# Kernel optimization log

Hardware: AMD Instinct MI355X
Metric: run time of the kernel (lower is better)

The kernel has to match this reference:

```python
import jax, jax.numpy as jnp
import numpy as np

D_E, D_ENC, D_DEC, H = 128, 256, 512, 8
HD = D_DEC // H
B, S, T, V, C = 32, 128, 128, 32000, 2


def gru_cell(x, h, Wih, Whh, bih, bhh):
    # PyTorch GRU cell: gates ordered (reset, update, new)
    gi = x @ Wih.T + bih
    gh = h @ Whh.T + bhh
    ir, iz, inn = jnp.split(gi, 3, axis=-1)
    hr, hz, hn = jnp.split(gh, 3, axis=-1)
    r = jax.nn.sigmoid(ir + hr)
    z = jax.nn.sigmoid(iz + hz)
    n = jnp.tanh(inn + r * hn)
    return (1.0 - z) * n + z * h


def setup_inputs():
    key = jax.random.key(0)
    ks = iter(jax.random.split(key, 40))
    def nrm(shape, s=0.05):
        return jax.random.normal(next(ks), shape, jnp.float32) * s
    inp = {}
    inp["nx"] = jax.random.randint(next(ks), (B, S), 0, V)
    inp["x"] = jax.random.randint(next(ks), (B, T), 0, V)
    inp["label"] = jax.random.randint(next(ks), (B,), 0, C)
    inp["tok_emb"] = nrm((V, D_E))
    inp["start_emb"] = nrm((1, D_E))
    inp["style_emb"] = nrm((C, D_DEC))
    for d in ("f", "b"):
        inp["enc_Wih_" + d] = nrm((3 * D_ENC, D_E))
        inp["enc_Whh_" + d] = nrm((3 * D_ENC, D_ENC))
        inp["enc_bih_" + d] = nrm((3 * D_ENC,))
        inp["enc_bhh_" + d] = nrm((3 * D_ENC,))
    inp["dec_Wih"] = nrm((3 * D_DEC, D_E))
    inp["dec_Whh"] = nrm((3 * D_DEC, D_DEC))
    inp["dec_bih"] = nrm((3 * D_DEC,))
    inp["dec_bhh"] = nrm((3 * D_DEC,))
    inp["attn_in_w"] = nrm((3 * D_DEC, D_DEC))
    inp["attn_in_b"] = nrm((3 * D_DEC,))
    inp["attn_out_w"] = nrm((D_DEC, D_DEC))
    inp["attn_out_b"] = nrm((D_DEC,))
    inp["ln_g"] = jnp.ones((D_DEC,), jnp.float32)
    inp["ln_b"] = jnp.zeros((D_DEC,), jnp.float32)
    inp["proj_w"] = nrm((V, D_DEC))
    inp["proj_b"] = nrm((V,))
    return inp


def _forward(nx, x, label, tok_emb, start_emb, style_emb,
             enc_Wih_f, enc_Whh_f, enc_bih_f, enc_bhh_f,
             enc_Wih_b, enc_Whh_b, enc_bih_b, enc_bhh_b,
             dec_Wih, dec_Whh, dec_bih, dec_bhh,
             attn_in_w, attn_in_b, attn_out_w, attn_out_b,
             ln_g, ln_b, proj_w, proj_b):
    b, s = nx.shape
    # --- bidirectional GRU encoder (dropout in eval mode => identity) ---
    emb = tok_emb[nx]                          # [B,S,dE]
    xs = jnp.swapaxes(emb, 0, 1)               # [S,B,dE]
    h0 = jnp.zeros((b, D_ENC), emb.dtype)

    def step_f(h, xt):
        h2 = gru_cell(xt, h, enc_Wih_f, enc_Whh_f, enc_bih_f, enc_bhh_f)
        return h2, h2

    def step_b(h, xt):
        h2 = gru_cell(xt, h, enc_Wih_b, enc_Whh_b, enc_bih_b, enc_bhh_b)
        return h2, h2

    _, out_f = jax.lax.scan(step_f, h0, xs)
    _, out_b = jax.lax.scan(step_b, h0, xs, reverse=True)
    memory = jnp.concatenate([out_f, out_b], axis=-1)   # [S,B,dDec] (seq-first, matches torch MHA)

    # --- precompute K/V projections of memory (invariant across decode steps) ---
    Wq, Wk, Wv = jnp.split(attn_in_w, 3, axis=0)
    bq, bk, bv = jnp.split(attn_in_b, 3)
    k = (memory @ Wk.T + bk).reshape(s, b, H, HD).transpose(1, 2, 0, 3)  # [B,H,S,HD]
    v = (memory @ Wv.T + bv).reshape(s, b, H, HD).transpose(1, 2, 0, 3)

    # --- teacher-forced decoder inputs: <start>, x[:,0], ..., x[:,T-2] ---
    dec_in = jnp.concatenate(
        [jnp.broadcast_to(start_emb[None, :, :], (b, 1, D_E)), tok_emb[x[:, :-1]]], axis=1)
    dec_xs = jnp.swapaxes(dec_in, 0, 1)        # [T,B,dE]
    h_init = style_emb[label]                  # [B,dDec]
    scale = 1.0 / np.sqrt(HD).astype(np.float32)

    def dec_step(h, xt):
        h_dec = gru_cell(xt, h, dec_Wih, dec_Whh, dec_bih, dec_bhh)      # [B,dDec]
        q = (h_dec @ Wq.T + bq).reshape(b, H, HD)
        scores = jnp.einsum('bhd,bhsd->bhs', q, k) * scale
        attn = jax.nn.softmax(scores, axis=-1)
        ctx = jnp.einsum('bhs,bhsd->bhd', attn, v).reshape(b, D_DEC)
        c = ctx @ attn_out_w.T + attn_out_b
        y = h_dec + c
        mu = jnp.mean(y, axis=-1, keepdims=True)
        var = jnp.var(y, axis=-1, keepdims=True)
        h_new = (y - mu) / jnp.sqrt(var + 1e-5) * ln_g + ln_b            # LayerNorm
        logits = h_new @ proj_w.T + proj_b                               # [B,V]
        return h_new, logits

    _, logits = jax.lax.scan(dec_step, h_init, dec_xs)   # [T,B,V]
    return jnp.swapaxes(logits, 0, 1)                    # [B,T,V]


def reference(nx, x, label, tok_emb, start_emb, style_emb,
              enc_Wih_f, enc_Whh_f, enc_bih_f, enc_bhh_f,
              enc_Wih_b, enc_Whh_b, enc_bih_b, enc_bhh_b,
              dec_Wih, dec_Whh, dec_bih, dec_bhh,
              attn_in_w, attn_in_b, attn_out_w, attn_out_b,
              ln_g, ln_b, proj_w, proj_b):
    return _forward(nx, x, label, tok_emb, start_emb, style_emb,
                    enc_Wih_f, enc_Whh_f, enc_bih_f, enc_bhh_f,
                    enc_Wih_b, enc_Whh_b, enc_bih_b, enc_bhh_b,
                    dec_Wih, dec_Whh, dec_bih, dec_bhh,
                    attn_in_w, attn_in_b, attn_out_w, attn_out_b,
                    ln_g, ln_b, proj_w, proj_b)
```

## Files before the change

### kernel.cpp

```cpp
#include <hip/hip_runtime.h>
#include <math.h>

typedef float f4 __attribute__((ext_vector_type(4)));
typedef short short8 __attribute__((ext_vector_type(8)));
typedef unsigned short us4 __attribute__((ext_vector_type(4)));

#define DEV static __device__ __forceinline__
#define AGENT __HIP_MEMORY_SCOPE_AGENT

DEV float bf2f(unsigned short u){ unsigned int x=((unsigned int)u)<<16; float f; __builtin_memcpy(&f,&x,4); return f; }
DEV unsigned short f2bf(float f){ unsigned int x; __builtin_memcpy(&x,&f,4); return (unsigned short)((x + 0x7fffu + ((x>>16)&1u))>>16); }

struct bfpair { short hi, lo; };
DEV bfpair splitbf(float v){
  bfpair p;
  unsigned short h_ = f2bf(v);
  p.hi = (short)h_;
  p.lo = (short)f2bf(v - bf2f(h_));
  return p;
}

DEV unsigned long long ldA64(const void* p){
  return __hip_atomic_load((const unsigned long long*)p, __ATOMIC_RELAXED, AGENT);
}
DEV void f2of(unsigned long long q, float* f0, float* f1){
  unsigned int lo=(unsigned int)q, hi=(unsigned int)(q>>32);
  __builtin_memcpy(f0,&lo,4); __builtin_memcpy(f1,&hi,4);
}

DEV void ld8x16_sc(const void* p, f4* o){
  asm volatile(
    "global_load_dwordx4 %0, %8, off sc0 sc1\n\t"
    "global_load_dwordx4 %1, %8, off offset:16 sc0 sc1\n\t"
    "global_load_dwordx4 %2, %8, off offset:32 sc0 sc1\n\t"
    "global_load_dwordx4 %3, %8, off offset:48 sc0 sc1\n\t"
    "global_load_dwordx4 %4, %8, off offset:64 sc0 sc1\n\t"
    "global_load_dwordx4 %5, %8, off offset:80 sc0 sc1\n\t"
    "global_load_dwordx4 %6, %8, off offset:96 sc0 sc1\n\t"
    "global_load_dwordx4 %7, %8, off offset:112 sc0 sc1\n\t"
    "s_waitcnt vmcnt(0)"
    : "=&v"(o[0]),"=&v"(o[1]),"=&v"(o[2]),"=&v"(o[3]),
      "=&v"(o[4]),"=&v"(o[5]),"=&v"(o[6]),"=&v"(o[7])
    : "v"(p) : "memory");
}
DEV void ld16x16_sc(const void* p, f4* o){
  asm volatile(
    "global_load_dwordx4 %0, %16, off sc0 sc1\n\t"
    "global_load_dwordx4 %1, %16, off offset:16 sc0 sc1\n\t"
    "global_load_dwordx4 %2, %16, off offset:32 sc0 sc1\n\t"
    "global_load_dwordx4 %3, %16, off offset:48 sc0 sc1\n\t"
    "global_load_dwordx4 %4, %16, off offset:64 sc0 sc1\n\t"
    "global_load_dwordx4 %5, %16, off offset:80 sc0 sc1\n\t"
    "global_load_dwordx4 %6, %16, off offset:96 sc0 sc1\n\t"
    "global_load_dwordx4 %7, %16, off offset:112 sc0 sc1\n\t"
    "global_load_dwordx4 %8, %16, off offset:128 sc0 sc1\n\t"
    "global_load_dwordx4 %9, %16, off offset:144 sc0 sc1\n\t"
    "global_load_dwordx4 %10, %16, off offset:160 sc0 sc1\n\t"
    "global_load_dwordx4 %11, %16, off offset:176 sc0 sc1\n\t"
    "global_load_dwordx4 %12, %16, off offset:192 sc0 sc1\n\t"
    "global_load_dwordx4 %13, %16, off offset:208 sc0 sc1\n\t"
    "global_load_dwordx4 %14, %16, off offset:224 sc0 sc1\n\t"
    "global_load_dwordx4 %15, %16, off offset:240 sc0 sc1\n\t"
    "s_waitcnt vmcnt(0)"
    : "=&v"(o[0]),"=&v"(o[1]),"=&v"(o[2]),"=&v"(o[3]),
      "=&v"(o[4]),"=&v"(o[5]),"=&v"(o[6]),"=&v"(o[7]),
      "=&v"(o[8]),"=&v"(o[9]),"=&v"(o[10]),"=&v"(o[11]),
      "=&v"(o[12]),"=&v"(o[13]),"=&v"(o[14]),"=&v"(o[15])
    : "v"(p) : "memory");
}
DEV void st8x16_sc(void* p, const f4* v){
  asm volatile(
    "global_store_dwordx4 %8, %0, off sc0 sc1\n\t"
    "global_store_dwordx4 %8, %1, off offset:16 sc0 sc1\n\t"
    "global_store_dwordx4 %8, %2, off offset:32 sc0 sc1\n\t"
    "global_store_dwordx4 %8, %3, off offset:48 sc0 sc1\n\t"
    "global_store_dwordx4 %8, %4, off offset:64 sc0 sc1\n\t"
    "global_store_dwordx4 %8, %5, off offset:80 sc0 sc1\n\t"
    "global_store_dwordx4 %8, %6, off offset:96 sc0 sc1\n\t"
    "global_store_dwordx4 %8, %7, off offset:112 sc0 sc1\n\t"
    "s_waitcnt vmcnt(0)"
    :: "v"(v[0]),"v"(v[1]),"v"(v[2]),"v"(v[3]),
       "v"(v[4]),"v"(v[5]),"v"(v[6]),"v"(v[7]),"v"(p) : "memory");
}

DEV int lds_off(int row,int strideShorts,int kShort){
  return row*strideShorts*2 + ((((kShort & ~7)*2) ^ ((row & 7)<<4)) + (kShort & 7)*2);
}
DEV void st8(unsigned short* lds,int row,int strideShorts,int k0,short8 v){
  *(short8*)((char*)lds + lds_off(row,strideShorts,k0)) = v;
}
DEV short8 ldfrag(const unsigned short* lds,int rowBase,int strideShorts,int k0){
  int lane = (int)(threadIdx.x & 63u);
  int row = rowBase + (lane & 15);
  int k = k0 + (lane >> 4)*8;
  return *(const short8*)((const char*)lds + lds_off(row,strideShorts,k));
}

DEV float dot8(f4 a0, f4 a1, short8 w){
  return a0[0]*bf2f((unsigned short)w[0]) + a0[1]*bf2f((unsigned short)w[1])
       + a0[2]*bf2f((unsigned short)w[2]) + a0[3]*bf2f((unsigned short)w[3])
       + a1[0]*bf2f((unsigned short)w[4]) + a1[1]*bf2f((unsigned short)w[5])
       + a1[2]*bf2f((unsigned short)w[6]) + a1[3]*bf2f((unsigned short)w[7]);
}

DEV void gbar_slot(int* slot, int nwg){
  __syncthreads();
  if (threadIdx.x==0){
    __hip_atomic_fetch_add(slot,1,__ATOMIC_RELAXED,AGENT);
    while (__hip_atomic_load(slot,__ATOMIC_RELAXED,AGENT) < nwg){
      __builtin_amdgcn_s_sleep(2);
    }
  }
  __syncthreads();
}

DEV void dbar(int* ctrs, int wg, int target){
  __syncthreads();
  if (threadIdx.x < 64){
    if (threadIdx.x == 0)
      __hip_atomic_store(&ctrs[wg*32], target, __ATOMIC_RELAXED, AGENT);
    for(;;){
      int v = __hip_atomic_load(&ctrs[(int)threadIdx.x*32], __ATOMIC_RELAXED, AGENT);
      if (__all(v >= target)) break;
      __builtin_amdgcn_s_sleep(2);
    }
  }
  __syncthreads();
}
DEV void vwait(int* ctrs, int target){
  if (threadIdx.x < 64){
    for(;;){
      int v = __hip_atomic_load(&ctrs[(int)threadIdx.x*32], __ATOMIC_RELAXED, AGENT);
      if (__all(v >= target)) break;
      __builtin_amdgcn_s_sleep(32);
    }
  }
  __syncthreads();
}
DEV void cwait(int* cctrs, int target){
  if (threadIdx.x < 64){
    for(;;){
      int v = __hip_atomic_load(&cctrs[((int)threadIdx.x & 7)*32], __ATOMIC_RELAXED, AGENT);
      if (__all(v >= target)) break;
      __builtin_amdgcn_s_sleep(32);
    }
  }
  __syncthreads();
}

__global__ void cvt_kernel(const float* __restrict__ src, unsigned short* __restrict__ dst, int n4){
  int stride = gridDim.x*blockDim.x;
  for (long i = blockIdx.x*blockDim.x + threadIdx.x; i < n4; i += stride){
    f4 v = *(const f4*)(src + i*4);
    us4 o; o[0]=f2bf(v[0]); o[1]=f2bf(v[1]); o[2]=f2bf(v[2]); o[3]=f2bf(v[3]);
    *(us4*)(dst + i*4) = o;
  }
}

__global__ void embed_kernel(const int* __restrict__ nx, const int* __restrict__ x,
  const int* __restrict__ label, const float* __restrict__ tok,
  const float* __restrict__ start, const float* __restrict__ style,
  unsigned short* __restrict__ embE, unsigned short* __restrict__ embD,
  float* __restrict__ h0)
{
  const int half = 4096*32;
  int i = blockIdx.x*256 + threadIdx.x;
  if (i < 2*half){
    const bool dec = i >= half;
    int j = dec ? i - half : i;
    int m = j >> 5, c4 = j & 31;
    int b = m & 31, tt = m >> 5;
    const float* src;
    if (!dec) src = tok + (long)nx[b*128 + tt]*128;
    else src = (tt == 0) ? start : (tok + (long)x[b*128 + tt - 1]*128);
    f4 v = *(const f4*)(src + c4*4);
    us4 o; o[0]=f2bf(v[0]); o[1]=f2bf(v[1]); o[2]=f2bf(v[2]); o[3]=f2bf(v[3]);
    *(us4*)((dec ? embD : embE) + (long)m*128 + c4*4) = o;
  } else {
    int j = i - 2*half;
    if (j < 4096){
      int b = j >> 7, c4 = j & 127;
      *(f4*)(h0 + b*512 + c4*4) = *(const f4*)(style + (long)label[b]*512 + c4*4);
    }
  }
}

__global__ void kv_reshape(const float* __restrict__ kvp, unsigned short* __restrict__ Kb, unsigned short* __restrict__ Vb){
  long i = (long)blockIdx.x*256 + threadIdx.x;
  if (i >= (long)4096*1024) return;
  int m = (int)(i >> 10), n = (int)(i & 1023);
  int s = m >> 5, b = m & 31;
  unsigned short bv = f2bf(kvp[i]);
  if (n < 512){
    int hh = n >> 6, d = n & 63;
    Kb[((long)(b*8 + hh)*128 + s)*64 + d] = bv;
  } else {
    int n2 = n - 512; int hh = n2 >> 6, d = n2 & 63;
    Vb[((long)(b*8 + hh)*64 + d)*128 + s] = bv;
  }
}

template<int MODE>
__global__ __launch_bounds__(256,2) void gemm64(
  const unsigned short* __restrict__ Bw, const float* __restrict__ bias,
  float* __restrict__ C, int M, int N, int K, int ldC,
  const unsigned short* __restrict__ Abf,
  const float* __restrict__ Af0, const float* __restrict__ Af1)
{
  __shared__ unsigned short a_s[64*64];
  __shared__ unsigned short b_s[64*64];
  const int tid = threadIdx.x, lane = tid & 63, wv = tid >> 6;
  const long mb = (long)blockIdx.x*64, nb = (long)blockIdx.y*64;
  f4 z = {0.f,0.f,0.f,0.f};
  f4 acc[4] = {z,z,z,z};
  const int r = tid >> 2, q = tid & 3, k0 = q*16;
  for (int kb = 0; kb < K; kb += 64){
    if (MODE==0){
      const unsigned short* src = Abf + (mb + r)*K + kb + k0;
      st8(a_s, r, 64, k0,   *(const short8*)src);
      st8(a_s, r, 64, k0+8, *(const short8*)(src+8));
    } else {
      float tmp[16];
      long m = mb + r;
      int kg = kb + k0;
      const float* base = (kg < 256) ? (Af0 + m*256 + kg) : (Af1 + m*256 + (kg - 256));
      #pragma unroll
      for (int i=0;i<16;i++) tmp[i] = base[i];
      short8 v0, v1;
      #pragma unroll
      for (int i=0;i<8;i++){ v0[i] = (short)f2bf(tmp[i]); v1[i] = (short)f2bf(tmp[8+i]); }
      st8(a_s, r, 64, k0, v0); st8(a_s, r, 64, k0+8, v1);
    }
    {
      const unsigned short* src = Bw + (nb + r)*K + kb + k0;
      st8(b_s, r, 64, k0,   *(const short8*)src);
      st8(b_s, r, 64, k0+8, *(const short8*)(src+8));
    }
    __syncthreads();
    #pragma unroll
    for (int kf=0; kf<2; kf++){
      short8 bfr = ldfrag(b_s, wv*16, 64, kf*32);
      #pragma unroll
      for (int mt=0; mt<4; mt++){
        short8 afr = ldfrag(a_s, mt*16, 64, kf*32);
        acc[mt] = __builtin_amdgcn_mfma_f32_16x16x32_bf16(afr, bfr, acc[mt], 0,0,0);
      }
    }
    __syncthreads();
  }
  const long col = nb + wv*16 + (lane & 15);
  const float bs = bias[col];
  #pragma unroll
  for (int mt=0; mt<4; mt++){
    #pragma unroll
    for (int rr=0; rr<4; rr++){
      long row = mb + mt*16 + (lane>>4)*4 + rr;
      C[row*(long)ldC + col] = acc[mt][rr] + bs;
    }
  }
}

__global__ __launch_bounds__(384) void enc_kernel(
  const float* __restrict__ WhhF_f, const float* __restrict__ WhhB_f,
  const float* __restrict__ GIF, const float* __restrict__ GIB,
  const float* __restrict__ bhhF, const float* __restrict__ bhhB,
  float* __restrict__ OUTF, float* __restrict__ OUTB,
  float* __restrict__ Hf,
  int* bar)
{
  __shared__ unsigned short whh_hi[96*256];
  __shared__ unsigned short whh_lo[96*256];
  __shared__ unsigned short a_hi[32*256];
  __shared__ unsigned short a_lo[32*256];
  __shared__ float ghscr[32*96];
  const int tid = threadIdx.x;
  const int wg = blockIdx.x;
  const int dir = wg >> 3, wgl = wg & 7;
  const float* Whh_f = dir ? WhhB_f : WhhF_f;
  const float* GI = dir ? GIB : GIF;
  const float* bhh = dir ? bhhB : bhhF;
  float* OUT = dir ? OUTB : OUTF;

  for (int idx = tid; idx < 96*32; idx += 384){
    int lr = idx >> 5, ch = idx & 31;
    int g_ = lr >> 5, jj = lr & 31;
    const float* wsrc = Whh_f + (long)(g_*256 + wgl*32 + jj)*256 + ch*8;
    short8 vh, vl;
    #pragma unroll
    for (int i=0;i<8;i++){ bfpair p = splitbf(wsrc[i]); vh[i] = p.hi; vl[i] = p.lo; }
    st8(whh_hi, lr, 256, ch*8, vh);
    st8(whh_lo, lr, 256, ch*8, vl);
  }
  __syncthreads();
  for (int t = 0; t < 128; t++){
    const int s = dir ? (127 - t) : t;
    const float* hbr = Hf + ((size_t)((t&1)*2 + dir))*(32*256);
    float* hbw = Hf + ((size_t)(((t+1)&1)*2 + dir))*(32*256);
    if (tid < 256){
      int b = tid >> 3, kg = tid & 7;
      const unsigned long long* hs = (const unsigned long long*)(hbr + b*256 + kg*32);
      #pragma unroll
      for (int c=0;c<4;c++){
        short8 vh, vl;
        #pragma unroll
        for (int i2=0;i2<4;i2++){
          unsigned long long qv = ldA64(hs + c*4 + i2);
          float f0, f1; f2of(qv, &f0, &f1);
          bfpair p0 = splitbf(f0), p1 = splitbf(f1);
          vh[i2*2] = p0.hi; vl[i2*2] = p0.lo;
          vh[i2*2+1] = p1.hi; vl[i2*2+1] = p1.lo;
        }
        st8(a_hi, b, 256, kg*32 + c*8, vh);
        st8(a_lo, b, 256, kg*32 + c*8, vl);
      }
    }
    __syncthreads();
    {
      const int wv = tid >> 6;
      f4 acc0 = {0.f,0.f,0.f,0.f}, acc1 = {0.f,0.f,0.f,0.f};
      #pragma unroll
      for (int kf=0; kf<8; kf++){
        short8 bhi = ldfrag(whh_hi, wv*16, 256, kf*32);
        short8 blo = ldfrag(whh_lo, wv*16, 256, kf*32);
        short8 ah0 = ldfrag(a_hi, 0, 256, kf*32);
        short8 al0 = ldfrag(a_lo, 0, 256, kf*32);
        short8 ah1 = ldfrag(a_hi, 16, 256, kf*32);
        short8 al1 = ldfrag(a_lo, 16, 256, kf*32);
        acc0 = __builtin_amdgcn_mfma_f32_16x16x32_bf16(ah0, bhi, acc0, 0,0,0);
        acc0 = __builtin_amdgcn_mfma_f32_16x16x32_bf16(al0, bhi, acc0, 0,0,0);
        acc0 = __builtin_amdgcn_mfma_f32_16x16x32_bf16(ah0, blo, acc0, 0,0,0);
        acc1 = __builtin_amdgcn_mfma_f32_16x16x32_bf16(ah1, bhi, acc1, 0,0,0);
        acc1 = __builtin_amdgcn_mfma_f32_16x16x32_bf16(al1, bhi, acc1, 0,0,0);
        acc1 = __builtin_amdgcn_mfma_f32_16x16x32_bf16(ah1, blo, acc1, 0,0,0);
      }
      const int lane = tid & 63;
      const int cl = wv*16 + (lane & 15);
      #pragma unroll
      for (int rr=0; rr<4; rr++){
        int r0 = (lane>>4)*4 + rr;
        ghscr[r0*96 + cl] = acc0[rr];
        ghscr[(16+r0)*96 + cl] = acc1[rr];
      }
    }
    __syncthreads();
    for (int task = tid; task < 1024; task += 384){
      int b = task >> 5, jj = task & 31;
      int jg = wgl*32 + jj;
      float ghr = ghscr[b*96 + jj]      + bhh[jg];
      float ghz = ghscr[b*96 + 32 + jj] + bhh[256 + jg];
      float ghn = ghscr[b*96 + 64 + jj] + bhh[512 + jg];
      const float* gi = GI + ((long)s*32 + b)*768;
      float r_ = 1.f/(1.f + __expf(-(gi[jg] + ghr)));
      float z_ = 1.f/(1.f + __expf(-(gi[256+jg] + ghz)));
      float n_ = tanhf(gi[512+jg] + r_*ghn);
      float hp = __hip_atomic_load(&hbr[b*256 + jg], __ATOMIC_RELAXED, AGENT);
      float hn = (1.f - z_)*n_ + z_*hp;
      OUT[((long)s*32 + b)*256 + jg] = hn;
      __hip_atomic_store(&hbw[b*256 + jg], hn, __ATOMIC_RELAXED, AGENT);
    }
    gbar_slot(bar + dir*128 + t, 8);
  }
}

struct DecS {
  unsigned short whh_hi[32*512];
  unsigned short whh_lo[32*512];
  unsigned short a_hi[32*512];
  unsigned short a_lo[32*512];
  float scr[32*64];
  float attn_l[4*128];
  float ctxs[4*64];
  float redm[32*8*2];
  float murs[64];
  float hnfr[32*8];
  float lngl[512], lnbl[512];
  float s1l[24], s2l[24];
};
struct VocS {
  unsigned short a_s[128*512];
  unsigned short b_s[64*64];
  float gl[512];
  float s2g[176];
};
struct CvtS {
  float redm[32*8*2];
  float murs[64];
};
union SU { DecS d; VocS v; CvtS c; };

__global__ __launch_bounds__(256,1) void dec_fused(
  const float* __restrict__ Whh_f,
  const unsigned short* __restrict__ WqBf,
  const unsigned short* __restrict__ Wout,
  const unsigned short* __restrict__ Kbf,
  const unsigned short* __restrict__ Vbf,
  const float* __restrict__ GI,
  const float* __restrict__ bhh,
  const float* __restrict__ aib,
  const float* __restrict__ aob,
  const float* __restrict__ lng,
  const float* __restrict__ lnb,
  const float* __restrict__ h0,
  float* __restrict__ Y,
  unsigned int* __restrict__ hdec32,
  unsigned short* __restrict__ Ybf,
  const unsigned short* __restrict__ Pbf,
  const float* __restrict__ projWf,
  const float* __restrict__ projB,
  float* __restrict__ out,
  int* ctrs)
{
  __shared__ SU s;
  const int tid = threadIdx.x;
  const int lane = tid & 63, wv = tid >> 6;
  int* cctrs = ctrs + 2048;

  if (blockIdx.x < 64){
    const int wg = blockIdx.x;
    const int h = wg >> 3, bg = wg & 7;
    const int jbase = wg*8;
    const int cw = wg & 7;

    if (tid < 24){ s.d.s1l[tid] = 0.f; s.d.s2l[tid] = 0.f; }
    __syncthreads();
    for (int idx = tid; idx < 32*64; idx += 256){
      int lr = idx >> 6, ch = idx & 63;
      short8 vh = {0,0,0,0,0,0,0,0}, vl = {0,0,0,0,0,0,0,0};
      if (lr < 24){
        int g_ = lr >> 3, jj = lr & 7;
        const float* wsrc = Whh_f + (long)(g_*512 + jbase + jj)*512 + ch*8;
        float s1p = 0.f, s2p = 0.f;
        #pragma unroll
        for (int i=0;i<8;i++){
          float wvv = wsrc[i];
          float gv = lng[ch*8+i];
          float bv = lnb[ch*8+i];
          float wp = wvv*gv;
          bfpair p = splitbf(wp);
          vh[i] = p.hi; vl[i] = p.lo;
          s1p += wp; s2p += bv*wvv;
        }
        atomicAdd(&s.d.s1l[lr], s1p);
        atomicAdd(&s.d.s2l[lr], s2p);
      }
      st8(s.d.whh_hi, lr, 512, ch*8, vh);
      st8(s.d.whh_lo, lr, 512, ch*8, vl);
    }
    for (int i = tid; i < 512; i += 256){ s.d.lngl[i] = lng[i]; s.d.lnbl[i] = lnb[i]; }

    const int qrow = h*64 + wv*16 + (lane & 15);
    const int kb0q = (lane>>4)*8;
    const unsigned short* wqbase = WqBf + (long)qrow*512 + kb0q;
    const int b_l = wv;
    const int bglob = bg*4 + b_l;
    const unsigned short* kbase = Kbf + ((long)(bglob*8 + h)*128 + lane*2)*64;
    const unsigned short* vbase = Vbf + ((long)(bglob*8 + h)*64 + lane)*128;
    const int jp = tid & 127;
    const unsigned short* wobase = Wout + (long)(jp*4)*512 + h*64;
    const float qb = aib[h*64 + wv*16 + (lane & 15)];
    const int bA = tid >> 3, kgA = tid & 7;
    const int jjA = tid & 7;
    const int jgA = jbase + jjA;
    const float bhr = bhh[jgA], bhz = bhh[512 + jgA], bhn = bhh[1024 + jgA];
    const float aobv = aob[jgA];
    __syncthreads();

    int lgen = 0;
    for (int t = 0; t < 128; t++){
      float gir = GI[((long)t*32 + bA)*1536 + jgA];
      float giz = GI[((long)t*32 + bA)*1536 + 512 + jgA];
      float gin = GI[((long)t*32 + bA)*1536 + 1024 + jgA];
      if (t == 0){
        const float* src = h0 + bA*512 + kgA*64;
        #pragma unroll
        for (int c=0;c<8;c++){
          short8 vh, vl;
          #pragma unroll
          for (int i=0;i<8;i++){
            float v = src[c*8+i];
            float gv = s.d.lngl[kgA*64 + c*8 + i];
            bfpair p = splitbf(v/gv);
            vh[i] = p.hi; vl[i] = p.lo;
            if (kgA == h && c == cw) s.d.hnfr[bA*8+i] = v;
          }
          st8(s.d.a_hi, bA, 512, kgA*64 + c*8, vh);
          st8(s.d.a_lo, bA, 512, kgA*64 + c*8, vl);
        }
        __syncthreads();
      } else {
        f4 yv[16];
        ld16x16_sc(Y + ((long)(t-1)*32 + bA)*512 + kgA*64, yv);
        float sm = 0.f, sq = 0.f;
        #pragma unroll
        for (int c=0;c<8;c++){
          short8 vh, vl;
          #pragma unroll
          for (int e=0;e<8;e++){
            float f = yv[c*2 + (e>>2)][e&3];
            sm += f; sq += f*f;
            bfpair p = splitbf(f);
            vh[e] = p.hi; vl[e] = p.lo;
            if (kgA == h && c == cw) s.d.hnfr[bA*8+e] = f;
          }
          st8(s.d.a_hi, bA, 512, kgA*64 + c*8, vh);
          st8(s.d.a_lo, bA, 512, kgA*64 + c*8, vl);
        }
        s.d.redm[(bA*8+kgA)*2] = sm; s.d.redm[(bA*8+kgA)*2+1] = sq;
        __syncthreads();
        if (tid < 32){
          float S1=0.f, S2=0.f;
          #pragma unroll
          for (int i=0;i<8;i++){ S1 += s.d.redm[(tid*8+i)*2]; S2 += s.d.redm[(tid*8+i)*2+1]; }
          float mu = S1*(1.f/512.f);
          float var = S2*(1.f/512.f) - mu*mu;
          s.d.murs[tid*2] = mu; s.d.murs[tid*2+1] = rsqrtf(var + 1e-5f);
        }
        __syncthreads();
      }
      {
        const int mt = wv >> 1, nt = wv & 1;
        f4 acc = {0.f,0.f,0.f,0.f};
        #pragma unroll
        for (int kf=0; kf<16; kf++){
          short8 bhi = ldfrag(s.d.whh_hi, nt*16, 512, kf*32);
          short8 blo = ldfrag(s.d.whh_lo, nt*16, 512, kf*32);
          short8 ahi = ldfrag(s.d.a_hi, mt*16, 512, kf*32);
          short8 alo = ldfrag(s.d.a_lo, mt*16, 512, kf*32);
          acc = __builtin_amdgcn_mfma_f32_16x16x32_bf16(ahi, bhi, acc, 0,0,0);
          acc = __builtin_amdgcn_mfma_f32_16x16x32_bf16(alo, bhi, acc, 0,0,0);
          acc = __builtin_amdgcn_mfma_f32_16x16x32_bf16(ahi, blo, acc, 0,0,0);
        }
        const int cl = nt*16 + (lane & 15);
        if (cl < 24){
          #pragma unroll
          for (int rr=0; rr<4; rr++){
            int row = mt*16 + (lane>>4)*4 + rr;
            s.d.scr[row*32 + cl] = acc[rr];
          }
        }
      }
      __syncthreads();
      {
        const float mu = t ? s.d.murs[bA*2] : 0.f;
        const float rsv = t ? s.d.murs[bA*2+1] : 1.f;
        const float c2 = rsv*mu;
        float ghr = rsv*s.d.scr[bA*32 + jjA]      - c2*s.d.s1l[jjA]      + (t ? s.d.s2l[jjA]      : 0.f) + bhr;
        float ghz = rsv*s.d.scr[bA*32 + 8 + jjA]  - c2*s.d.s1l[8 + jjA]  + (t ? s.d.s2l[8 + jjA]  : 0.f) + bhz;
        float ghn = rsv*s.d.scr[bA*32 + 16 + jjA] - c2*s.d.s1l[16 + jjA] + (t ? s.d.s2l[16 + jjA] : 0.f) + bhn;
        float r_ = 1.f/(1.f + __expf(-(gir + ghr)));
        float z_ = 1.f/(1.f + __expf(-(giz + ghz)));
        float n_ = tanhf(gin + r_*ghn);
        float hpv = s.d.hnfr[bA*8 + jjA];
        float hp = t ? (hpv - mu)*rsv*s.d.lngl[jgA] + s.d.lnbl[jgA] : hpv;
        float hd = (1.f - z_)*n_ + z_*hp;
        unsigned int hb = (unsigned int)f2bf(hd);
        unsigned int other = (unsigned int)__shfl_xor((int)hb, 1);
        if ((jjA & 1) == 0){
          unsigned int pack = hb | (other << 16);
          __hip_atomic_store(&hdec32[bA*256 + (jgA >> 1)], pack, __ATOMIC_RELAXED, AGENT);
        }
        __hip_atomic_store(&Y[((long)t*32 + bA)*512 + jgA], hd + aobv, __ATOMIC_RELAXED, AGENT);
      }
      dbar(ctrs, wg, ++lgen);
      {
        f4 hv[8];
        ld8x16_sc(hdec32 + bA*256 + kgA*32, hv);
        #pragma unroll
        for (int c=0;c<8;c++){
          short8 v;
          #pragma unroll
          for (int w2=0; w2<4; w2++){
            float fv = hv[c][w2];
            unsigned int u; __builtin_memcpy(&u, &fv, 4);
            v[w2*2]   = (short)(u & 0xffff);
            v[w2*2+1] = (short)(u >> 16);
          }
          st8(s.d.a_hi, bA, 512, kgA*64 + c*8, v);
        }
      }
      __syncthreads();
      {
        f4 acc0 = {0.f,0.f,0.f,0.f}, acc1 = {0.f,0.f,0.f,0.f};
        #pragma unroll
        for (int kf=0; kf<16; kf++){
          short8 bfr = *(const short8*)(wqbase + kf*32);
          acc0 = __builtin_amdgcn_mfma_f32_16x16x32_bf16(ldfrag(s.d.a_hi, 0, 512, kf*32), bfr, acc0, 0,0,0);
          acc1 = __builtin_amdgcn_mfma_f32_16x16x32_bf16(ldfrag(s.d.a_hi, 16, 512, kf*32), bfr, acc1, 0,0,0);
        }
        const int cl = wv*16 + (lane & 15);
        #pragma unroll
        for (int rr=0; rr<4; rr++){
          int r0 = (lane>>4)*4 + rr;
          s.d.scr[r0*64 + cl] = acc0[rr] + qb;
          s.d.scr[(16+r0)*64 + cl] = acc1[rr] + qb;
        }
      }
      __syncthreads();
      {
        const f4* qp = (const f4*)(s.d.scr + bglob*64);
        float s0 = 0.f, s1 = 0.f;
        #pragma unroll
        for (int c=0;c<8;c++) s0 += dot8(qp[c*2], qp[c*2+1], *(const short8*)(kbase + c*8));
        #pragma unroll
        for (int c=0;c<8;c++) s1 += dot8(qp[c*2], qp[c*2+1], *(const short8*)(kbase + 64 + c*8));
        s0 *= 0.125f; s1 *= 0.125f;
        float mx = fmaxf(s0, s1);
        #pragma unroll
        for (int o=1;o<64;o<<=1) mx = fmaxf(mx, __shfl_xor(mx, o));
        float e0 = __expf(s0 - mx), e1 = __expf(s1 - mx);
        float sm = e0 + e1;
        #pragma unroll
        for (int o=1;o<64;o<<=1) sm += __shfl_xor(sm, o);
        float inv = 1.f/sm;
        s.d.attn_l[b_l*128 + lane*2]   = e0*inv;
        s.d.attn_l[b_l*128 + lane*2+1] = e1*inv;
      }
      __syncthreads();
      {
        const f4* ap = (const f4*)(s.d.attn_l + b_l*128);
        float cx = 0.f;
        #pragma unroll
        for (int c=0;c<16;c++) cx += dot8(ap[c*2], ap[c*2+1], *(const short8*)(vbase + c*8));
        s.d.ctxs[b_l*64 + lane] = cx;
      }
      __syncthreads();
      {
        const int b2 = tid >> 7;
        #pragma unroll
        for (int jj=0;jj<4;jj++){
          const unsigned short* wb = wobase + (long)jj*512;
          short8 w0 = *(const short8*)(wb);
          short8 w1 = *(const short8*)(wb+8);
          short8 w2 = *(const short8*)(wb+16);
          short8 w3 = *(const short8*)(wb+24);
          short8 w4 = *(const short8*)(wb+32);
          short8 w5 = *(const short8*)(wb+40);
          short8 w6 = *(const short8*)(wb+48);
          short8 w7 = *(const short8*)(wb+56);
          #pragma unroll
          for (int bb=0; bb<2; bb++){
            const int bl = b2 + bb*2;
            const int bgl = bg*4 + bl;
            const f4* cp = (const f4*)(s.d.ctxs + bl*64);
            float cj = dot8(cp[0], cp[1], w0) + dot8(cp[2], cp[3], w1)
                     + dot8(cp[4], cp[5], w2) + dot8(cp[6], cp[7], w3)
                     + dot8(cp[8], cp[9], w4) + dot8(cp[10], cp[11], w5)
                     + dot8(cp[12], cp[13], w6) + dot8(cp[14], cp[15], w7);
            atomicAdd(&Y[((long)t*32 + bgl)*512 + jp*4 + jj], cj);
          }
        }
      }
      dbar(ctrs, wg, ++lgen);
    }
  } else if (blockIdx.x < 72){
    const int w = blockIdx.x - 64;
    const int rr = tid >> 3, seg = tid & 7;
    for (int c = 0; c < 16; c++){
      vwait(ctrs, 16*(c+1));
      long m = (long)c*256 + w*32 + rr;
      f4 yv[16];
      ld16x16_sc(Y + m*512 + seg*64, yv);
      float sm = 0.f, sq = 0.f;
      #pragma unroll
      for (int i=0;i<16;i++){
        f4 v = yv[i];
        sm += v[0]+v[1]+v[2]+v[3];
        sq += v[0]*v[0]+v[1]*v[1]+v[2]*v[2]+v[3]*v[3];
      }
      s.c.redm[(rr*8+seg)*2] = sm; s.c.redm[(rr*8+seg)*2+1] = sq;
      __syncthreads();
      if (tid < 32){
        float S1=0.f, S2=0.f;
        #pragma unroll
        for (int i=0;i<8;i++){ S1 += s.c.redm[(tid*8+i)*2]; S2 += s.c.redm[(tid*8+i)*2+1]; }
        float mu = S1*(1.f/512.f);
        float var = S2*(1.f/512.f) - mu*mu;
        s.c.murs[tid*2] = mu; s.c.murs[tid*2+1] = rsqrtf(var + 1e-5f);
      }
      __syncthreads();
      const float mu = s.c.murs[rr*2], rsv = s.c.murs[rr*2+1];
      f4 ob[8];
      #pragma unroll
      for (int i2=0;i2<32;i2++){
        float a0 = (yv[(2*i2)>>2][(2*i2)&3] - mu)*rsv;
        float a1v = (yv[(2*i2+1)>>2][(2*i2+1)&3] - mu)*rsv;
        unsigned int u = (unsigned int)f2bf(a0) | ((unsigned int)f2bf(a1v)<<16);
        float uf; __builtin_memcpy(&uf,&u,4);
        ob[i2>>2][i2&3] = uf;
      }
      st8x16_sc(Ybf + m*512 + seg*64, ob);
      __syncthreads();
      if (tid == 0)
        __hip_atomic_store(&cctrs[w*32], c+1, __ATOMIC_RELAXED, AGENT);
    }
  } else {
    const int w2 = blockIdx.x - 72;
    const int c0 = w2*174;
    const int cn = (32000 - c0 < 174) ? (32000 - c0) : 174;
    for (int cc = tid; cc < 176; cc += 256){
      if (cc < cn){
        const float* pw = projWf + (long)(c0+cc)*512;
        float s2 = 0.f;
        for (int k=0;k<512;k++) s2 += lnb[k]*pw[k];
        s.v.s2g[cc] = s2;
      }
    }
    for (int i = tid; i < 512; i += 256) s.v.gl[i] = lng[i];
    __syncthreads();
    const f4 z4 = {0.f,0.f,0.f,0.f};
    for (int c=0; c<16; c++){
      cwait(cctrs, c+1);
      for (int half=0; half<2; half++){
        const long rbase = (long)c*256 + half*128;
        {
          const int row = tid >> 1, seg = tid & 1;
          const unsigned short* src = Ybf + (rbase + row)*512 + seg*256;
          #pragma unroll
          for (int blk=0; blk<2; blk++){
            f4 av[16];
            ld16x16_sc(src + blk*128, av);
            #pragma unroll
            for (int i=0;i<16;i++){
              f4 tv = av[i];
              short8 s8; __builtin_memcpy(&s8, &tv, 16);
              st8(s.v.a_s, row, 512, seg*256 + blk*128 + i*8, s8);
            }
          }
        }
        __syncthreads();
        for (int nt=0; nt<3; nt++){
          f4 acc[8] = {z4,z4,z4,z4,z4,z4,z4,z4};
          for (int kt=0; kt<8; kt++){
            {
              const int r = tid >> 2, q = tid & 3, k0 = q*16;
              const int col = nt*64 + r;
              short8 v0 = {0,0,0,0,0,0,0,0}, v1 = {0,0,0,0,0,0,0,0};
              if (col < cn){
                const unsigned short* src = Pbf + (long)(c0+col)*512 + kt*64 + k0;
                #pragma unroll
                for (int i=0;i<8;i++){
                  v0[i] = (short)f2bf(bf2f(src[i])   * s.v.gl[kt*64 + k0 + i]);
                  v1[i] = (short)f2bf(bf2f(src[8+i]) * s.v.gl[kt*64 + k0 + 8 + i]);
                }
              }
              st8(s.v.b_s, r, 64, k0, v0);
              st8(s.v.b_s, r, 64, k0+8, v1);
            }
            __syncthreads();
            #pragma unroll
            for (int kf=0; kf<2; kf++){
              short8 bfr = ldfrag(s.v.b_s, wv*16, 64, kf*32);
              #pragma unroll
              for (int mt=0; mt<8; mt++){
                short8 afr = ldfrag(s.v.a_s, mt*16, 512, kt*64 + kf*32);
                acc[mt] = __builtin_amdgcn_mfma_f32_16x16x32_bf16(afr, bfr, acc[mt], 0,0,0);
              }
            }
            __syncthreads();
          }
          const int colloc = nt*64 + wv*16 + (lane & 15);
          if (colloc < cn){
            const int vcol = c0 + colloc;
            const float corr = s.v.s2g[colloc] + projB[vcol];
            #pragma unroll
            for (int mt=0; mt<8; mt++){
              #pragma unroll
              for (int rr=0; rr<4; rr++){
                int rowl = mt*16 + (lane>>4)*4 + rr;
                long m = rbase + rowl;
                long tt = m >> 5, b = m & 31;
                out[(b*128 + tt)*32000 + vcol] = acc[mt][rr] + corr;
              }
            }
          }
        }
        __syncthreads();
      }
    }
  }
}

extern "C" void kernel_launch(void* const* d_in, const int* in_sizes, int n_in,
                              void* d_out, int out_size, void* d_ws, size_t ws_size,
                              hipStream_t stream)
{
  const int* nx = (const int*)d_in[0];
  const int* x = (const int*)d_in[1];
  const int* label = (const int*)d_in[2];
  const float* tok = (const float*)d_in[3];
  const float* start = (const float*)d_in[4];
  const float* style = (const float*)d_in[5];
  const float* eWihF = (const float*)d_in[6];
  const float* eWhhF = (const float*)d_in[7];
  const float* ebihF = (const float*)d_in[8];
  const float* ebhhF = (const float*)d_in[9];
  const float* eWihB = (const float*)d_in[10];
  const float* eWhhB = (const float*)d_in[11];
  const float* ebihB = (const float*)d_in[12];
  const float* ebhhB = (const float*)d_in[13];
  const float* dWih = (const float*)d_in[14];
  const float* dWhh = (const float*)d_in[15];
  const float* dbih = (const float*)d_in[16];
  const float* dbhh = (const float*)d_in[17];
  const float* ainW = (const float*)d_in[18];
  const float* ainB = (const float*)d_in[19];
  const float* aoutW = (const float*)d_in[20];
  const float* aoutB = (const float*)d_in[21];
  const float* lng = (const float*)d_in[22];
  const float* lnb = (const float*)d_in[23];
  const float* projW = (const float*)d_in[24];
  const float* projB = (const float*)d_in[25];
  float* out = (float*)d_out;
  char* W = (char*)d_ws;

  size_t off = 0;
  auto alloc = [&](size_t sz){ size_t o = off; off = (off + sz + 255) & ~(size_t)255; return o; };
  const size_t O_HF   = alloc(4*32*256*4);
  const size_t O_BAR  = alloc(16384);
  const size_t O_EIHF = alloc(768*128*2);
  const size_t O_EIHB = alloc(768*128*2);
  const size_t O_DIH  = alloc(1536*128*2);
  const size_t O_AIN  = alloc(1536*512*2);
  const size_t O_AOUT = alloc(512*512*2);
  const size_t O_PROJ = alloc((size_t)32000*512*2);
  const size_t O_EMBE = alloc(4096*128*2);
  const size_t O_EMBD = alloc(4096*128*2);
  const size_t O_KBF  = alloc((size_t)32*8*128*64*2);
  const size_t O_VBF  = alloc((size_t)32*8*128*64*2);
  const size_t O_HDEC = alloc(32*256*4);
  const size_t O_YBF  = alloc((size_t)4096*512*2);
  const size_t O_GIF  = alloc((size_t)4096*768*4);
  const size_t O_GIB  = alloc((size_t)4096*768*4);
  const size_t O_GID  = alloc((size_t)4096*1536*4);
  const size_t O_OUTF = alloc((size_t)4096*256*4);
  const size_t O_OUTB = alloc((size_t)4096*256*4);
  const size_t O_KVP  = alloc((size_t)4096*1024*4);
  const size_t O_Y    = alloc((size_t)4096*512*4);
  const size_t O_H0   = alloc(32*512*4);

  (void)hipMemsetAsync(W + O_HF, 0, (O_BAR - O_HF) + 16384, stream);

  auto US = [&](size_t o){ return (unsigned short*)(W + o); };
  auto FP = [&](size_t o){ return (float*)(W + o); };

  {
    const struct { const float* s; size_t d; int n; } cvs[] = {
      {eWihF, O_EIHF, 768*128}, {eWihB, O_EIHB, 768*128},
      {dWih,  O_DIH,  1536*128},
      {ainW,  O_AIN,  1536*512}, {aoutW, O_AOUT, 512*512},
      {projW, O_PROJ, 32000*512},
    };
    for (auto &c : cvs){
      int n4 = c.n/4;
      int blocks = (n4 + 255)/256; if (blocks > 4096) blocks = 4096;
      cvt_kernel<<<blocks, 256, 0, stream>>>(c.s, US(c.d), n4);
    }
  }
  embed_kernel<<<1040, 256, 0, stream>>>(nx, x, label, tok, start, style,
                                         US(O_EMBE), US(O_EMBD), FP(O_H0));
  gemm64<0><<<dim3(64,12), 256, 0, stream>>>(US(O_EIHF), ebihF, FP(O_GIF), 4096, 768, 128, 768,
                                             US(O_EMBE), nullptr, nullptr);
  gemm64<0><<<dim3(64,12), 256, 0, stream>>>(US(O_EIHB), ebihB, FP(O_GIB), 4096, 768, 128, 768,
                                             US(O_EMBE), nullptr, nullptr);
  gemm64<0><<<dim3(64,24), 256, 0, stream>>>(US(O_DIH), dbih, FP(O_GID), 4096, 1536, 128, 1536,
                                             US(O_EMBD), nullptr, nullptr);
  enc_kernel<<<16, 384, 0, stream>>>(eWhhF, eWhhB, FP(O_GIF), FP(O_GIB),
                                     ebhhF, ebhhB, FP(O_OUTF), FP(O_OUTB), FP(O_HF),
                                     (int*)(W + O_BAR) + 3072);
  gemm64<1><<<dim3(64,16), 256, 0, stream>>>(US(O_AIN) + 512*512, ainB + 512, FP(O_KVP),
                                             4096, 1024, 512, 1024,
                                             nullptr, FP(O_OUTF), FP(O_OUTB));
  kv_reshape<<<16384, 256, 0, stream>>>(FP(O_KVP), US(O_KBF), US(O_VBF));
  dec_fused<<<256, 256, 0, stream>>>(dWhh, US(O_AIN), US(O_AOUT), US(O_KBF), US(O_VBF),
                                     FP(O_GID), dbhh, ainB, aoutB, lng, lnb, FP(O_H0),
                                     FP(O_Y), (unsigned int*)(W + O_HDEC), US(O_YBF),
                                     US(O_PROJ), projW, projB, out,
                                     (int*)(W + O_BAR));
  (void)in_sizes; (void)n_in; (void)out_size; (void)ws_size;
}
```

Baseline: 4.503 ms.

## Compute attention queries only for the block's own batches and prefetch GI

```diff
diff --git a/kernel.cpp b/kernel.cpp
--- a/kernel.cpp
+++ b/kernel.cpp
@@ -28,6 +28,12 @@
   __builtin_memcpy(f0,&lo,4); __builtin_memcpy(f1,&hi,4);
 }
 
+DEV void ld1x16_sc(const void* p, f4* o){
+  asm volatile(
+    "global_load_dwordx4 %0, %1, off sc0 sc1\n\t"
+    "s_waitcnt vmcnt(0)"
+    : "=&v"(o[0]) : "v"(p) : "memory");
+}
 DEV void ld8x16_sc(const void* p, f4* o){
   asm volatile(
     "global_load_dwordx4 %0, %8, off sc0 sc1\n\t"
@@ -132,7 +138,7 @@
     for(;;){
       int v = __hip_atomic_load(&ctrs[(int)threadIdx.x*32], __ATOMIC_RELAXED, AGENT);
       if (__all(v >= target)) break;
-      __builtin_amdgcn_s_sleep(32);
+      __builtin_amdgcn_s_sleep(64);
     }
   }
   __syncthreads();
@@ -142,7 +148,7 @@
     for(;;){
       int v = __hip_atomic_load(&cctrs[((int)threadIdx.x & 7)*32], __ATOMIC_RELAXED, AGENT);
       if (__all(v >= target)) break;
-      __builtin_amdgcn_s_sleep(32);
+      __builtin_amdgcn_s_sleep(64);
     }
   }
   __syncthreads();
@@ -466,10 +472,10 @@
     __syncthreads();
 
     int lgen = 0;
+    float gir = GI[((long)0*32 + bA)*1536 + jgA];
+    float giz = GI[((long)0*32 + bA)*1536 + 512 + jgA];
+    float gin = GI[((long)0*32 + bA)*1536 + 1024 + jgA];
     for (int t = 0; t < 128; t++){
-      float gir = GI[((long)t*32 + bA)*1536 + jgA];
-      float giz = GI[((long)t*32 + bA)*1536 + 512 + jgA];
-      float gin = GI[((long)t*32 + bA)*1536 + 1024 + jgA];
       if (t == 0){
         const float* src = h0 + bA*512 + kgA*64;
         #pragma unroll
@@ -563,41 +569,37 @@
       }
       dbar(ctrs, wg, ++lgen);
       {
-        f4 hv[8];
-        ld8x16_sc(hdec32 + bA*256 + kgA*32, hv);
-        #pragma unroll
-        for (int c=0;c<8;c++){
-          short8 v;
-          #pragma unroll
-          for (int w2=0; w2<4; w2++){
-            float fv = hv[c][w2];
-            unsigned int u; __builtin_memcpy(&u, &fv, 4);
-            v[w2*2]   = (short)(u & 0xffff);
-            v[w2*2+1] = (short)(u >> 16);
-          }
-          st8(s.d.a_hi, bA, 512, kgA*64 + c*8, v);
-        }
+        const int r4 = tid >> 6, ch = tid & 63;
+        f4 hv;
+        ld1x16_sc(hdec32 + (bg*4 + r4)*256 + ch*4, &hv);
+        short8 v;
+        #pragma unroll
+        for (int w2=0; w2<4; w2++){
+          float fv = hv[w2];
+          unsigned int u; __builtin_memcpy(&u, &fv, 4);
+          v[w2*2]   = (short)(u & 0xffff);
+          v[w2*2+1] = (short)(u >> 16);
+        }
+        st8(s.d.a_hi, r4, 512, ch*8, v);
       }
       __syncthreads();
       {
-        f4 acc0 = {0.f,0.f,0.f,0.f}, acc1 = {0.f,0.f,0.f,0.f};
+        f4 acc0 = {0.f,0.f,0.f,0.f};
         #pragma unroll
         for (int kf=0; kf<16; kf++){
           short8 bfr = *(const short8*)(wqbase + kf*32);
           acc0 = __builtin_amdgcn_mfma_f32_16x16x32_bf16(ldfrag(s.d.a_hi, 0, 512, kf*32), bfr, acc0, 0,0,0);
-          acc1 = __builtin_amdgcn_mfma_f32_16x16x32_bf16(ldfrag(s.d.a_hi, 16, 512, kf*32), bfr, acc1, 0,0,0);
         }
         const int cl = wv*16 + (lane & 15);
-        #pragma unroll
-        for (int rr=0; rr<4; rr++){
-          int r0 = (lane>>4)*4 + rr;
-          s.d.scr[r0*64 + cl] = acc0[rr] + qb;
-          s.d.scr[(16+r0)*64 + cl] = acc1[rr] + qb;
+        if ((lane >> 4) == 0){
+          #pragma unroll
+          for (int rr=0; rr<4; rr++)
+            s.d.scr[rr*64 + cl] = acc0[rr] + qb;
         }
       }
       __syncthreads();
       {
-        const f4* qp = (const f4*)(s.d.scr + bglob*64);
+        const f4* qp = (const f4*)(s.d.scr + b_l*64);
         float s0 = 0.f, s1 = 0.f;
         #pragma unroll
         for (int c=0;c<8;c++) s0 += dot8(qp[c*2], qp[c*2+1], *(const short8*)(kbase + c*8));
@@ -649,6 +651,12 @@
             atomicAdd(&Y[((long)t*32 + bgl)*512 + jp*4 + jj], cj);
           }
         }
+      }
+      if (t < 127){
+        long base = ((long)(t+1)*32 + bA)*1536 + jgA;
+        gir = GI[base];
+        giz = GI[base + 512];
+        gin = GI[base + 1024];
       }
       dbar(ctrs, wg, ++lgen);
     }
```

New measurement: 3.852 ms. 14.5% less time.
